# Kernel optimization log

Hardware: AMD Instinct MI355X
Metric: run time of the kernel (lower is better)

The kernel has to match this reference:

```python
import jax, jax.numpy as jnp
import numpy as np


def setup_inputs() -> dict:
    key = jax.random.key(0)
    ks = jax.random.split(key, 15)
    B, r, d, h, na = 64, 64, 2048, 64, 256
    x = jax.random.normal(ks[0], (B, d, na), dtype=jnp.float32)
    L = jax.random.randint(ks[1], (B, 2, na), 0, 2).astype(jnp.float32)
    p = lambda i, shp: jax.random.normal(ks[i], shp, dtype=jnp.float32)
    return {
        "x": x, "L": L,
        "Aq": p(2, (r, d)), "Ak": p(3, (r, d)), "Av": p(4, (r, d)),
        "Aq1": p(5, (r, r)), "Ak1": p(6, (r, r)), "Av1": p(7, (r, r)),
        "Aq5": p(8, (r, r)), "Ak5": p(9, (r, r)), "Av5": p(10, (r, r)),
        "Ao": p(11, (r, r)), "Ao1": p(12, (r, r)), "Ao5": p(13, (h, r)),
    }


def reference(x, L, Aq, Ak, Av, Aq1, Ak1, Av1, Aq5, Ak5, Av5, Ao, Ao1, Ao5):
    B, d, na = x.shape
    # numNeighbors: count of L[:,0,:] >= 1 per batch, +1 -> [B,1,1]
    numN = jnp.sum((L[:, 0, :] >= 1.0).astype(jnp.float32), axis=1)[:, None, None] + 1.0
    scale = jnp.sqrt(numN)  # [B,1,1]

    def attn(M, Wq, Wk, Wv):
        # M: [B, f, na]; Wq/Wk/Wv: [r, f]
        Q = jax.nn.sigmoid(jnp.einsum('rf,bfn->bnr', Wq, M))  # [B,na,r]
        K = jax.nn.sigmoid(jnp.einsum('rf,bfn->brn', Wk, M))  # [B,r,na]
        V = jax.nn.sigmoid(jnp.einsum('rf,bfn->bnr', Wv, M))  # [B,na,r]
        A = jax.nn.softmax(jnp.einsum('bnr,brm->bnm', Q, K) / scale, axis=2)
        return jnp.einsum('bnm,bmr->brn', A, V)  # [B,r,na]

    o = attn(x, Aq, Ak, Av)
    M = jax.nn.silu(jnp.einsum('sr,brn->bsn', Ao, o))
    o = attn(M, Aq1, Ak1, Av1)
    M = jax.nn.silu(jnp.einsum('sr,brn->bsn', Ao1, o))
    o = attn(M, Aq5, Ak5, Av5)
    M = jax.nn.silu(jnp.einsum('hr,brn->bhn', Ao5, o))  # [B,h,na]

    blk = d // na  # rows per block (8)
    def diagvec(i):
        # kron(sum-of-squares, ones(1,2)) == repeat each element twice -> [B, 2*na]
        return jnp.repeat(jnp.sum(M[:, i * blk:(i + 1) * blk, :] ** 2, axis=1), 2, axis=1)

    M11, M12, M21, M22 = diagvec(0), diagvec(1), diagvec(2), diagvec(3)
    Mpp = jnp.sum(M[:, 4 * blk:, :] ** 2, axis=1)  # [B, na]

    # q = x[:, :4, :].transpose(1,2).reshape(B, 4*na) (agent-major ordering)
    q = jnp.transpose(x[:, :4, :], (0, 2, 1)).reshape(B, 4 * na)
    q1, q2 = q[:, :2 * na], q[:, 2 * na:]
    # Block matrix [[diag(M11), diag(M12)], [diag(M21), diag(M22)]] quadratic form,
    # computed without materializing the [B, 4na, 4na] matrix.
    quad = jnp.sum(M11 * q1 * q1 + M12 * q1 * q2 + M21 * q2 * q1 + M22 * q2 * q2,
                   axis=1, keepdims=True)
    return quad + jnp.sum(Mpp, axis=1, keepdims=True)  # [B, 1]
```

## Files before the change

kernel.cpp:

```cpp
#include <hip/hip_runtime.h>
#include <stdint.h>

typedef _Float16 f16;
typedef f16 f16x8 __attribute__((ext_vector_type(8)));
typedef float f32x4 __attribute__((ext_vector_type(4)));

#define MFMA(a,b,c) __builtin_amdgcn_mfma_f32_16x16x32_f16(a, b, c, 0, 0, 0)

__device__ __forceinline__ float sigmoidf_(float z) { return 1.0f / (1.0f + __expf(-z)); }

__global__ void prep_kernel(const float* __restrict__ L,
    const float* __restrict__ Aq, const float* __restrict__ Ak, const float* __restrict__ Av,
    const float* __restrict__ Aq1, const float* __restrict__ Ak1, const float* __restrict__ Av1,
    const float* __restrict__ Aq5, const float* __restrict__ Ak5, const float* __restrict__ Av5,
    const float* __restrict__ Ao, const float* __restrict__ Ao1, const float* __restrict__ Ao5,
    float* __restrict__ scale, f16* __restrict__ Wcat, f16* __restrict__ Wsm,
    float* __restrict__ out)
{
  __shared__ float r4[4];
  int blk = blockIdx.x, t = threadIdx.x;
  if (blk < 64) {
    float v = (L[blk * 512 + t] >= 1.0f) ? 1.0f : 0.0f;
    #pragma unroll
    for (int off = 32; off; off >>= 1) v += __shfl_down(v, off);
    if ((t & 63) == 0) r4[t >> 6] = v;
    __syncthreads();
    if (t == 0) scale[blk] = sqrtf(r4[0] + r4[1] + r4[2] + r4[3] + 1.0f);
  } else if (blk < 160) {
    int base = (blk - 64) * 4096;
    for (int i = 0; i < 16; i++) {
      int idx = base + t + i * 256;
      int row = idx >> 11, col = idx & 2047;
      float v = (row < 64) ? Aq[row * 2048 + col]
              : (row < 128) ? Ak[(row - 64) * 2048 + col]
              : Av[(row - 128) * 2048 + col];
      Wcat[idx] = (f16)v;
    }
  } else if (blk < 169) {
    int j = blk - 160;
    const float* s = (j == 0) ? Aq1 : (j == 1) ? Ak1 : (j == 2) ? Av1 : (j == 3) ? Aq5
                   : (j == 4) ? Ak5 : (j == 5) ? Av5 : (j == 6) ? Ao : (j == 7) ? Ao1 : Ao5;
    for (int i = 0; i < 16; i++) { int idx = t + i * 256; Wsm[j * 4096 + idx] = (f16)s[idx]; }
  } else {
    if (t < 64) out[t] = 0.0f;
  }
}

__global__ __launch_bounds__(256) void qkv1_kernel(const float* __restrict__ x,
    const f16* __restrict__ Wcat, f16* __restrict__ Qt, f16* __restrict__ Kt,
    f16* __restrict__ Vg)
{
  int b = blockIdx.y, n0 = blockIdx.x * 32;
  int t = threadIdx.x, lane = t & 63, w = t >> 6;
  int l15 = lane & 15, q = lane >> 4;
  __shared__ f16 xt[32 * 72];
  __shared__ f16 wt[192 * 72];
  f32x4 acc[2][3] = {};
  const float* xb = x + (size_t)b * 524288 + n0;
  int tn = t & 31, fg = t >> 5;

  for (int f0 = 0; f0 < 2048; f0 += 64) {
    #pragma unroll
    for (int rep = 0; rep < 4; rep++) {
      int fl = fg * 8 + rep * 2;
      float a0 = xb[(size_t)(f0 + fl) * 256 + tn];
      float a1 = xb[(size_t)(f0 + fl + 1) * 256 + tn];
      uint32_t pk = (uint32_t)__builtin_bit_cast(uint16_t, (f16)a0)
                  | ((uint32_t)__builtin_bit_cast(uint16_t, (f16)a1) << 16);
      *(uint32_t*)&xt[tn * 72 + fl] = pk;
    }
    #pragma unroll
    for (int i = 0; i < 6; i++) {
      int id = t + i * 256, r = id >> 3, c = id & 7;
      *(uint4*)&wt[r * 72 + c * 8] = *(const uint4*)(Wcat + (size_t)r * 2048 + f0 + c * 8);
    }
    __syncthreads();
    #pragma unroll
    for (int ks = 0; ks < 2; ks++) {
      int k0 = ks * 32 + q * 8;
      f16x8 af[2], bf[3];
      af[0] = *(const f16x8*)&xt[l15 * 72 + k0];
      af[1] = *(const f16x8*)&xt[(16 + l15) * 72 + k0];
      #pragma unroll
      for (int j = 0; j < 3; j++) bf[j] = *(const f16x8*)&wt[((w * 3 + j) * 16 + l15) * 72 + k0];
      #pragma unroll
      for (int nt = 0; nt < 2; nt++)
        #pragma unroll
        for (int j = 0; j < 3; j++)
          acc[nt][j] = MFMA(af[nt], bf[j], acc[nt][j]);
    }
    __syncthreads();
  }
  #pragma unroll
  for (int nt = 0; nt < 2; nt++)
    #pragma unroll
    for (int j = 0; j < 3; j++) {
      int rr = (w * 3 + j) * 16 + l15;
      float s[4];
      #pragma unroll
      for (int reg = 0; reg < 4; reg++) s[reg] = sigmoidf_(acc[nt][j][reg]);
      int nbase = n0 + nt * 16 + q * 4;
      if (rr < 64) {
        #pragma unroll
        for (int reg = 0; reg < 4; reg++)
          Qt[(size_t)b * 16384 + (size_t)(nbase + reg) * 64 + rr] = (f16)s[reg];
      } else if (rr < 128) {
        #pragma unroll
        for (int reg = 0; reg < 4; reg++)
          Kt[(size_t)b * 16384 + (size_t)(nbase + reg) * 64 + (rr - 64)] = (f16)s[reg];
      } else {
        union { f16 h[4]; uint2 u; } pk;
        #pragma unroll
        for (int reg = 0; reg < 4; reg++) pk.h[reg] = (f16)s[reg];
        *(uint2*)(Vg + (size_t)b * 16384 + (size_t)(rr - 128) * 256 + nbase) = pk.u;
      }
    }
}

template<int LAYER>
__global__ __launch_bounds__(512) void attnB_kernel(const float* __restrict__ x,
    const float* __restrict__ scale, const f16* __restrict__ Wsm,
    const f16* __restrict__ Qtg, const f16* __restrict__ Ktg, const f16* __restrict__ Vgg,
    const f16* __restrict__ Min, f16* __restrict__ Mout, float* __restrict__ out)
{
  int g = blockIdx.x, b = blockIdx.y, n0 = g * 64;
  int t = threadIdx.x, lane = t & 63, w = t >> 6;
  int l15 = lane & 15, q = lane >> 4;
  __shared__ f16 KT[256 * 72];
  __shared__ f16 SM[256 * 72];
  __shared__ f16 VM[64 * 264];
  __shared__ f16 QT[64 * 72];
  __shared__ f16 OT[64 * 72];
  __shared__ float denomS[64];

  float sinv = 1.0f / scale[b];
  if (t < 64) denomS[t] = 0.0f;

  if (LAYER == 0) {
    const uint4* qs = (const uint4*)(Qtg + (size_t)b * 16384 + (size_t)n0 * 64);
    { int n = t >> 3, c = t & 7; *(uint4*)&QT[n * 72 + c * 8] = qs[t]; }
    const uint4* ks = (const uint4*)(Ktg + (size_t)b * 16384);
    const uint4* vs = (const uint4*)(Vgg + (size_t)b * 16384);
    #pragma unroll
    for (int i = 0; i < 4; i++) {
      int id = t + i * 512;
      int m = id >> 3, c = id & 7;
      *(uint4*)&KT[m * 72 + c * 8] = ks[id];
      int r = id >> 5, c2 = id & 31;
      *(uint4*)&VM[r * 264 + c2 * 8] = vs[id];
    }
  } else {
    const uint4* ms = (const uint4*)(Min + (size_t)b * 16384);
    #pragma unroll
    for (int i = 0; i < 4; i++) {
      int id = t + i * 512, m = id >> 3, c = id & 7;
      *(uint4*)&SM[m * 72 + c * 8] = ms[id];
    }
  }
  __syncthreads();

  const f16* Wq = Wsm + (size_t)(LAYER == 1 ? 0 : 3) * 4096;
  const f16* Wk = Wsm + (size_t)(LAYER == 1 ? 1 : 4) * 4096;
  const f16* Wv = Wsm + (size_t)(LAYER == 1 ? 2 : 5) * 4096;
  const f16* Wo = Wsm + (size_t)(LAYER == 0 ? 6 : (LAYER == 1 ? 7 : 8)) * 4096;

  if (LAYER > 0) {
    if (w < 4) {
      f16x8 bk[4][2];
      #pragma unroll
      for (int rt = 0; rt < 4; rt++) {
        bk[rt][0] = *(const f16x8*)(Wk + (rt * 16 + l15) * 64 + q * 8);
        bk[rt][1] = *(const f16x8*)(Wk + (rt * 16 + l15) * 64 + 32 + q * 8);
      }
      #pragma unroll
      for (int mi = 0; mi < 4; mi++) {
        int mt = w * 4 + mi;
        f16x8 a0 = *(const f16x8*)&SM[(mt * 16 + l15) * 72 + q * 8];
        f16x8 a1 = *(const f16x8*)&SM[(mt * 16 + l15) * 72 + 32 + q * 8];
        #pragma unroll
        for (int rt = 0; rt < 4; rt++) {
          f32x4 acc = {}; acc = MFMA(a0, bk[rt][0], acc); acc = MFMA(a1, bk[rt][1], acc);
          #pragma unroll
          for (int reg = 0; reg < 4; reg++)
            KT[(mt * 16 + q * 4 + reg) * 72 + rt * 16 + l15] = (f16)sigmoidf_(acc[reg]);
        }
      }
    } else {
      f16x8 av[4][2];
      #pragma unroll
      for (int rt = 0; rt < 4; rt++) {
        av[rt][0] = *(const f16x8*)(Wv + (rt * 16 + l15) * 64 + q * 8);
        av[rt][1] = *(const f16x8*)(Wv + (rt * 16 + l15) * 64 + 32 + q * 8);
      }
      #pragma unroll
      for (int mi = 0; mi < 4; mi++) {
        int mt = (w - 4) * 4 + mi;
        f16x8 b0 = *(const f16x8*)&SM[(mt * 16 + l15) * 72 + q * 8];
        f16x8 b1 = *(const f16x8*)&SM[(mt * 16 + l15) * 72 + 32 + q * 8];
        #pragma unroll
        for (int rt = 0; rt < 4; rt++) {
          f32x4 acc = {}; acc = MFMA(av[rt][0], b0, acc); acc = MFMA(av[rt][1], b1, acc);
          #pragma unroll
          for (int reg = 0; reg < 4; reg++)
            VM[(rt * 16 + q * 4 + reg) * 264 + mt * 16 + l15] = (f16)sigmoidf_(acc[reg]);
        }
      }
    }
    {
      int nt = w >> 1;
      f16x8 a0 = *(const f16x8*)&SM[(n0 + nt * 16 + l15) * 72 + q * 8];
      f16x8 a1 = *(const f16x8*)&SM[(n0 + nt * 16 + l15) * 72 + 32 + q * 8];
      #pragma unroll
      for (int j = 0; j < 2; j++) {
        int rt = (w & 1) * 2 + j;
        f16x8 b0 = *(const f16x8*)(Wq + (rt * 16 + l15) * 64 + q * 8);
        f16x8 b1 = *(const f16x8*)(Wq + (rt * 16 + l15) * 64 + 32 + q * 8);
        f32x4 acc = {}; acc = MFMA(a0, b0, acc); acc = MFMA(a1, b1, acc);
        #pragma unroll
        for (int reg = 0; reg < 4; reg++)
          QT[(nt * 16 + q * 4 + reg) * 72 + rt * 16 + l15] = (f16)sigmoidf_(acc[reg]);
      }
    }
    __syncthreads();
  }

  {
    int nt = w >> 1;
    f16x8 a0 = *(const f16x8*)&QT[(nt * 16 + l15) * 72 + q * 8];
    f16x8 a1 = *(const f16x8*)&QT[(nt * 16 + l15) * 72 + 32 + q * 8];
    float dsum[4] = {0.f, 0.f, 0.f, 0.f};
    #pragma unroll
    for (int mi = 0; mi < 8; mi++) {
      int mt = (w & 1) * 8 + mi;
      f16x8 b0 = *(const f16x8*)&KT[(mt * 16 + l15) * 72 + q * 8];
      f16x8 b1 = *(const f16x8*)&KT[(mt * 16 + l15) * 72 + 32 + q * 8];
      f32x4 acc = {}; acc = MFMA(a0, b0, acc); acc = MFMA(a1, b1, acc);
      #pragma unroll
      for (int reg = 0; reg < 4; reg++) {
        float e = __expf(acc[reg] * sinv);
        dsum[reg] += e;
        SM[(nt * 16 + q * 4 + reg) * 264 + mt * 16 + l15] = (f16)e;
      }
    }
    #pragma unroll
    for (int reg = 0; reg < 4; reg++) {
      #pragma unroll
      for (int mask = 1; mask < 16; mask <<= 1) dsum[reg] += __shfl_xor(dsum[reg], mask);
    }
    if (l15 == 0) {
      #pragma unroll
      for (int reg = 0; reg < 4; reg++) atomicAdd(&denomS[nt * 16 + q * 4 + reg], dsum[reg]);
    }
  }
  __syncthreads();

  {
    int nt = w >> 1;
    f32x4 oacc[2] = {};
    #pragma unroll
    for (int kc = 0; kc < 8; kc++) {
      f16x8 af = *(const f16x8*)&SM[(nt * 16 + l15) * 264 + kc * 32 + q * 8];
      #pragma unroll
      for (int j = 0; j < 2; j++) {
        int rt = (w & 1) * 2 + j;
        f16x8 bf = *(const f16x8*)&VM[(rt * 16 + l15) * 264 + kc * 32 + q * 8];
        oacc[j] = MFMA(af, bf, oacc[j]);
      }
    }
    #pragma unroll
    for (int j = 0; j < 2; j++) {
      int rt = (w & 1) * 2 + j;
      #pragma unroll
      for (int reg = 0; reg < 4; reg++) {
        int row = nt * 16 + q * 4 + reg;
        OT[row * 72 + rt * 16 + l15] = (f16)(oacc[j][reg] / denomS[row]);
      }
    }
  }
  __syncthreads();

  f16* Mst = QT;
  {
    int nt = w >> 1;
    f16x8 a0 = *(const f16x8*)&OT[(nt * 16 + l15) * 72 + q * 8];
    f16x8 a1 = *(const f16x8*)&OT[(nt * 16 + l15) * 72 + 32 + q * 8];
    #pragma unroll
    for (int j = 0; j < 2; j++) {
      int st = (w & 1) * 2 + j;
      f16x8 b0 = *(const f16x8*)(Wo + (st * 16 + l15) * 64 + q * 8);
      f16x8 b1 = *(const f16x8*)(Wo + (st * 16 + l15) * 64 + 32 + q * 8);
      f32x4 acc = {}; acc = MFMA(a0, b0, acc); acc = MFMA(a1, b1, acc);
      #pragma unroll
      for (int reg = 0; reg < 4; reg++) {
        float z = acc[reg];
        Mst[(nt * 16 + q * 4 + reg) * 64 + st * 16 + l15] = (f16)(z * sigmoidf_(z));
      }
    }
  }
  __syncthreads();

  if (LAYER < 2) {
    int row = t >> 3, c = t & 7;
    *(uint4*)(Mout + (size_t)b * 16384 + (size_t)(n0 + row) * 64 + c * 8)
        = *(const uint4*)&Mst[row * 64 + c * 8];
  } else {
    float contrib = 0.0f;
    if (t < 64) {
      int ntok = n0 + t;
      const f16* row = &Mst[t * 64];
      float d[4] = {0, 0, 0, 0}, pp = 0.0f;
      #pragma unroll
      for (int gg = 0; gg < 8; gg++) {
        f16x8 v = *(const f16x8*)(row + gg * 8);
        float ss = 0.0f;
        #pragma unroll
        for (int k = 0; k < 8; k++) { float f = (float)v[k]; ss += f * f; }
        if (gg < 4) d[gg] = ss; else pp += ss;
      }
      int np = ntok >> 1, c0 = (ntok & 1) * 2;
      const float* xb = x + (size_t)b * 524288 + (size_t)c0 * 256;
      float q1a = xb[np], q1b = xb[256 + np];
      float q2a = xb[128 + np], q2b = xb[384 + np];
      contrib = d[0] * (q1a * q1a + q1b * q1b)
              + (d[1] + d[2]) * (q1a * q2a + q1b * q2b)
              + d[3] * (q2a * q2a + q2b * q2b) + pp;
    }
    if (w == 0) {
      #pragma unroll
      for (int off = 32; off; off >>= 1) contrib += __shfl_down(contrib, off);
      if (lane == 0) atomicAdd(out + b, contrib);
    }
  }
}

extern "C" void kernel_launch(void* const* d_in, const int* in_sizes, int n_in,
                              void* d_out, int out_size, void* d_ws, size_t ws_size,
                              hipStream_t stream) {
  const float* x   = (const float*)d_in[0];
  const float* L   = (const float*)d_in[1];
  const float* Aq  = (const float*)d_in[2];
  const float* Ak  = (const float*)d_in[3];
  const float* Av  = (const float*)d_in[4];
  const float* Aq1 = (const float*)d_in[5];
  const float* Ak1 = (const float*)d_in[6];
  const float* Av1 = (const float*)d_in[7];
  const float* Aq5 = (const float*)d_in[8];
  const float* Ak5 = (const float*)d_in[9];
  const float* Av5 = (const float*)d_in[10];
  const float* Ao  = (const float*)d_in[11];
  const float* Ao1 = (const float*)d_in[12];
  const float* Ao5 = (const float*)d_in[13];

  char* ws = (char*)d_ws;
  float* scale = (float*)ws;
  f16* Wcat  = (f16*)(ws + 256);
  f16* Wsm   = (f16*)(ws + 786688);
  f16* Qtg   = (f16*)(ws + 860416);
  f16* Ktg   = (f16*)(ws + 2957568);
  f16* Vgg   = (f16*)(ws + 5054720);
  f16* MbufA = (f16*)(ws + 7151872);
  f16* MbufB = (f16*)(ws + 9249024);
  float* out = (float*)d_out;

  prep_kernel<<<170, 256, 0, stream>>>(L, Aq, Ak, Av, Aq1, Ak1, Av1,
                                       Aq5, Ak5, Av5, Ao, Ao1, Ao5, scale, Wcat, Wsm, out);
  qkv1_kernel<<<dim3(8, 64), 256, 0, stream>>>(x, Wcat, Qtg, Ktg, Vgg);
  attnB_kernel<0><<<dim3(4, 64), 512, 0, stream>>>(x, scale, Wsm, Qtg, Ktg, Vgg,
                                                   nullptr, MbufA, out);
  attnB_kernel<1><<<dim3(4, 64), 512, 0, stream>>>(x, scale, Wsm, Qtg, Ktg, Vgg,
                                                   MbufA, MbufB, out);
  attnB_kernel<2><<<dim3(4, 64), 512, 0, stream>>>(x, scale, Wsm, Qtg, Ktg, Vgg,
                                                   MbufB, nullptr, out);
}
```

Measured before the change: 271.3 us.

## Double-buffer QKV projection tiles in LDS and use fast reciprocals

The first-layer QKV projection kernel now double-buffers its x and weight tiles in shared memory. Global loads for the next K-chunk are issued into registers before the MFMAs on the current chunk and written to the other buffer afterwards, which leaves one barrier per iteration. This is meant to hide global-load latency behind the matrix math, at the cost of twice the LDS and more registers. Separately, the divisions in sigmoid, the score scale and the softmax normalisation are replaced with hardware approximate reciprocals and multiplies, which is slightly less precise.

```diff
diff --git a/kernel.cpp b/kernel.cpp
--- a/kernel.cpp
+++ b/kernel.cpp
@@ -7,7 +7,9 @@
 
 #define MFMA(a,b,c) __builtin_amdgcn_mfma_f32_16x16x32_f16(a, b, c, 0, 0, 0)
 
-__device__ __forceinline__ float sigmoidf_(float z) { return 1.0f / (1.0f + __expf(-z)); }
+__device__ __forceinline__ float sigmoidf_(float z) {
+  return __builtin_amdgcn_rcpf(1.0f + __expf(-z));
+}
 
 __global__ void prep_kernel(const float* __restrict__ L,
     const float* __restrict__ Aq, const float* __restrict__ Ak, const float* __restrict__ Av,
@@ -53,44 +55,89 @@
   int b = blockIdx.y, n0 = blockIdx.x * 32;
   int t = threadIdx.x, lane = t & 63, w = t >> 6;
   int l15 = lane & 15, q = lane >> 4;
-  __shared__ f16 xt[32 * 72];
-  __shared__ f16 wt[192 * 72];
+  __shared__ f16 xt[2][32 * 72];
+  __shared__ f16 wt[2][192 * 72];
   f32x4 acc[2][3] = {};
   const float* xb = x + (size_t)b * 524288 + n0;
   int tn = t & 31, fg = t >> 5;
 
+  int r0 = t >> 3,           c0 = t & 7;
+  int r1 = (t + 256) >> 3,   c1 = (t + 256) & 7;
+  int r2 = (t + 512) >> 3,   c2 = (t + 512) & 7;
+  int r3 = (t + 768) >> 3,   c3 = (t + 768) & 7;
+  int r4 = (t + 1024) >> 3,  c4 = (t + 1024) & 7;
+  int r5 = (t + 1280) >> 3,  c5 = (t + 1280) & 7;
+  const f16* pw0 = Wcat + (size_t)r0 * 2048 + c0 * 8;
+  const f16* pw1 = Wcat + (size_t)r1 * 2048 + c1 * 8;
+  const f16* pw2 = Wcat + (size_t)r2 * 2048 + c2 * 8;
+  const f16* pw3 = Wcat + (size_t)r3 * 2048 + c3 * 8;
+  const f16* pw4 = Wcat + (size_t)r4 * 2048 + c4 * 8;
+  const f16* pw5 = Wcat + (size_t)r5 * 2048 + c5 * 8;
+  const float* px = xb + (size_t)(fg * 8) * 256 + tn;
+
+  float xa0, xa1, xa2, xa3, xa4, xa5, xa6, xa7;
+  uint4 wr0, wr1, wr2, wr3, wr4, wr5;
+
+#define LOAD_X(f0n) do {                                                        \
+    const float* xp_ = px + (size_t)(f0n) * 256;                                \
+    xa0 = xp_[0];    xa1 = xp_[256];  xa2 = xp_[512];  xa3 = xp_[768];          \
+    xa4 = xp_[1024]; xa5 = xp_[1280]; xa6 = xp_[1536]; xa7 = xp_[1792];         \
+  } while (0)
+
+#define LOAD_W(f0n) do {                                                        \
+    wr0 = *(const uint4*)(pw0 + (f0n)); wr1 = *(const uint4*)(pw1 + (f0n));     \
+    wr2 = *(const uint4*)(pw2 + (f0n)); wr3 = *(const uint4*)(pw3 + (f0n));     \
+    wr4 = *(const uint4*)(pw4 + (f0n)); wr5 = *(const uint4*)(pw5 + (f0n));     \
+  } while (0)
+
+#define WRITE_XW(buf) do {                                                      \
+    f16x8 pk_;                                                                  \
+    pk_[0] = (f16)xa0; pk_[1] = (f16)xa1; pk_[2] = (f16)xa2; pk_[3] = (f16)xa3; \
+    pk_[4] = (f16)xa4; pk_[5] = (f16)xa5; pk_[6] = (f16)xa6; pk_[7] = (f16)xa7; \
+    *(f16x8*)&xt[buf][tn * 72 + fg * 8] = pk_;                                  \
+    f16* wb_ = &wt[buf][0];                                                     \
+    *(uint4*)&wb_[r0 * 72 + c0 * 8] = wr0;                                      \
+    *(uint4*)&wb_[r1 * 72 + c1 * 8] = wr1;                                      \
+    *(uint4*)&wb_[r2 * 72 + c2 * 8] = wr2;                                      \
+    *(uint4*)&wb_[r3 * 72 + c3 * 8] = wr3;                                      \
+    *(uint4*)&wb_[r4 * 72 + c4 * 8] = wr4;                                      \
+    *(uint4*)&wb_[r5 * 72 + c5 * 8] = wr5;                                      \
+  } while (0)
+
+  LOAD_X(0);
+  LOAD_W(0);
+  WRITE_XW(0);
+  __syncthreads();
+
+  int cur = 0;
   for (int f0 = 0; f0 < 2048; f0 += 64) {
-    #pragma unroll
-    for (int rep = 0; rep < 4; rep++) {
-      int fl = fg * 8 + rep * 2;
-      float a0 = xb[(size_t)(f0 + fl) * 256 + tn];
-      float a1 = xb[(size_t)(f0 + fl + 1) * 256 + tn];
-      uint32_t pk = (uint32_t)__builtin_bit_cast(uint16_t, (f16)a0)
-                  | ((uint32_t)__builtin_bit_cast(uint16_t, (f16)a1) << 16);
-      *(uint32_t*)&xt[tn * 72 + fl] = pk;
-    }
-    #pragma unroll
-    for (int i = 0; i < 6; i++) {
-      int id = t + i * 256, r = id >> 3, c = id & 7;
-      *(uint4*)&wt[r * 72 + c * 8] = *(const uint4*)(Wcat + (size_t)r * 2048 + f0 + c * 8);
-    }
-    __syncthreads();
+    int nxt = cur ^ 1;
+    bool more = (f0 + 64 < 2048);
+    if (more) { LOAD_X(f0 + 64); LOAD_W(f0 + 64); }
+
     #pragma unroll
     for (int ks = 0; ks < 2; ks++) {
       int k0 = ks * 32 + q * 8;
       f16x8 af[2], bf[3];
-      af[0] = *(const f16x8*)&xt[l15 * 72 + k0];
-      af[1] = *(const f16x8*)&xt[(16 + l15) * 72 + k0];
-      #pragma unroll
-      for (int j = 0; j < 3; j++) bf[j] = *(const f16x8*)&wt[((w * 3 + j) * 16 + l15) * 72 + k0];
+      af[0] = *(const f16x8*)&xt[cur][l15 * 72 + k0];
+      af[1] = *(const f16x8*)&xt[cur][(16 + l15) * 72 + k0];
+      #pragma unroll
+      for (int j = 0; j < 3; j++) bf[j] = *(const f16x8*)&wt[cur][((w * 3 + j) * 16 + l15) * 72 + k0];
       #pragma unroll
       for (int nt = 0; nt < 2; nt++)
         #pragma unroll
         for (int j = 0; j < 3; j++)
           acc[nt][j] = MFMA(af[nt], bf[j], acc[nt][j]);
     }
+
+    if (more) WRITE_XW(nxt);
     __syncthreads();
-  }
+    cur = nxt;
+  }
+#undef LOAD_X
+#undef LOAD_W
+#undef WRITE_XW
+
   #pragma unroll
   for (int nt = 0; nt < 2; nt++)
     #pragma unroll
@@ -133,7 +180,7 @@
   __shared__ f16 OT[64 * 72];
   __shared__ float denomS[64];
 
-  float sinv = 1.0f / scale[b];
+  float sinv = __builtin_amdgcn_rcpf(scale[b]);
   if (t < 64) denomS[t] = 0.0f;
 
   if (LAYER == 0) {
@@ -267,13 +314,17 @@
         oacc[j] = MFMA(af, bf, oacc[j]);
       }
     }
+    float rden[4];
+    #pragma unroll
+    for (int reg = 0; reg < 4; reg++)
+      rden[reg] = __builtin_amdgcn_rcpf(denomS[nt * 16 + q * 4 + reg]);
     #pragma unroll
     for (int j = 0; j < 2; j++) {
       int rt = (w & 1) * 2 + j;
       #pragma unroll
       for (int reg = 0; reg < 4; reg++) {
         int row = nt * 16 + q * 4 + reg;
-        OT[row * 72 + rt * 16 + l15] = (f16)(oacc[j][reg] / denomS[row]);
+        OT[row * 72 + rt * 16 + l15] = (f16)(oacc[j][reg] * rden[reg]);
       }
     }
   }
```

Measured after the change: 265.4 us. 1.02x faster.
